# Kernel tuning notes

Measured on AMD Instinct MI355X. Metric: run time of the kernel, lower is better.

## Reference

```python
import jax, jax.numpy as jnp
import numpy as np
import math

NUM_BINS = 10
TAIL_BOUND = 5.0
FILTER_CHANNELS = 192
KERNEL_SIZE = 3
N_LAYERS = 3
HALF = 1
MIN_BIN = 1e-3
MIN_DERIV = 1e-3


def conv1d(x, w, b, dilation=1, groups=1, padding=0):
    # x: [B,C,T], w: [O, C//groups, K]
    y = jax.lax.conv_general_dilated(
        x, w, window_strides=(1,), padding=[(padding, padding)],
        rhs_dilation=(dilation,), dimension_numbers=('NCH', 'OIH', 'NCH'),
        feature_group_count=groups)
    return y + b[None, :, None]


def ln_channels(x, g, b, eps=1e-5):
    # LayerNorm over channel dim (VITS modules.LayerNorm)
    m = jnp.mean(x, axis=1, keepdims=True)
    v = jnp.mean((x - m) ** 2, axis=1, keepdims=True)
    return g[None, :, None] * (x - m) * jax.lax.rsqrt(v + eps) + b[None, :, None]


def rq_spline(x1, uw, uh, ud):
    # piecewise rational-quadratic transform with linear tails (Durkan et al.)
    # x1: [B,1,T]; uw,uh: [B,1,T,K]; ud: [B,1,T,K-1]
    K = NUM_BINS
    tb = TAIL_BOUND
    inside = (x1 >= -tb) & (x1 <= tb)

    const = math.log(math.exp(1.0 - MIN_DERIV) - 1.0)  # softplus^-1(1-min_d)
    ud = jnp.pad(ud, [(0, 0)] * (ud.ndim - 1) + [(1, 1)], constant_values=const)

    widths = jax.nn.softmax(uw, axis=-1)
    widths = MIN_BIN + (1.0 - MIN_BIN * K) * widths
    cumw = jnp.pad(jnp.cumsum(widths, -1), [(0, 0)] * (uw.ndim - 1) + [(1, 0)])
    cumw = 2.0 * tb * cumw - tb
    cumw = cumw.at[..., 0].set(-tb).at[..., -1].set(tb)
    widths = cumw[..., 1:] - cumw[..., :-1]

    heights = jax.nn.softmax(uh, axis=-1)
    heights = MIN_BIN + (1.0 - MIN_BIN * K) * heights
    cumh = jnp.pad(jnp.cumsum(heights, -1), [(0, 0)] * (uh.ndim - 1) + [(1, 0)])
    cumh = 2.0 * tb * cumh - tb
    cumh = cumh.at[..., 0].set(-tb).at[..., -1].set(tb)
    heights = cumh[..., 1:] - cumh[..., :-1]

    derivs = MIN_DERIV + jax.nn.softplus(ud)  # [..., K+1]

    xin = jnp.clip(x1, -tb, tb)  # clamp so out-of-range lanes stay finite
    locs = cumw.at[..., -1].add(1e-6)
    bin_idx = jnp.clip(jnp.sum((xin[..., None] >= locs).astype(jnp.int32), -1) - 1, 0, K - 1)

    def take(a):
        return jnp.take_along_axis(a, bin_idx[..., None], axis=-1)[..., 0]

    icw = take(cumw)
    iw = take(widths)
    ich = take(cumh)
    ih = take(heights)
    d_l = take(derivs[..., :-1])
    d_r = take(derivs[..., 1:])
    delta = ih / iw

    theta = (xin - icw) / iw
    t1m = theta * (1.0 - theta)
    numerator = ih * (delta * theta * theta + d_l * t1m)
    denominator = delta + (d_l + d_r - 2.0 * delta) * t1m
    y = ich + numerator / denominator
    dnum = (delta * delta) * (d_r * theta * theta + 2.0 * delta * t1m + d_l * (1.0 - theta) ** 2)
    lad = jnp.log(dnum) - 2.0 * jnp.log(denominator)

    out = jnp.where(inside, y, x1)       # linear tails: identity outside
    lad = jnp.where(inside, lad, 0.0)
    return out, lad


def reference(x, x_mask, pre_w, pre_b, sep_w, sep_b, pw_w, pw_b,
              ln1_g, ln1_b, ln2_g, ln2_b, proj_w, proj_b):
    x0, x1 = x[:, :HALF], x[:, HALF:]
    h = conv1d(x0, pre_w, pre_b)
    # DDSConv (dilated depth-separable conv stack), p_dropout=0
    for i in range(N_LAYERS):
        d = KERNEL_SIZE ** i
        pad = (KERNEL_SIZE * d - d) // 2
        y = conv1d(h * x_mask, sep_w[i], sep_b[i], dilation=d,
                   groups=FILTER_CHANNELS, padding=pad)
        y = jax.nn.gelu(ln_channels(y, ln1_g[i], ln1_b[i]), approximate=False)
        y = conv1d(y, pw_w[i], pw_b[i])
        y = jax.nn.gelu(ln_channels(y, ln2_g[i], ln2_b[i]), approximate=False)
        h = h + y
    h = h * x_mask
    h = conv1d(h, proj_w, proj_b) * x_mask  # [B, half*(3K-1), T]
    b, c, t = x0.shape
    h = h.reshape(b, c, -1, t).transpose(0, 1, 3, 2)  # [B, half, T, 3K-1]
    scale = math.sqrt(FILTER_CHANNELS)
    uw = h[..., :NUM_BINS] / scale
    uh = h[..., NUM_BINS:2 * NUM_BINS] / scale
    ud = h[..., 2 * NUM_BINS:]
    x1o, lad = rq_spline(x1, uw, uh, ud)
    out = jnp.concatenate([x0, x1o], axis=1) * x_mask
    logdet = jnp.sum(lad * x_mask, axis=(1, 2))
    return out, logdet


def setup_inputs() -> dict:
    key = jax.random.key(0)
    ks = jax.random.split(key, 8)
    B, T, C, L, K = 64, 4096, FILTER_CHANNELS, N_LAYERS, KERNEL_SIZE
    return {
        'x': jax.random.normal(ks[0], (B, 2, T), jnp.float32),
        'x_mask': jnp.ones((B, 1, T), jnp.float32),
        'pre_w': jax.random.normal(ks[1], (C, 1, 1), jnp.float32) * 0.1,
        'pre_b': jnp.zeros((C,), jnp.float32),
        'sep_w': jax.random.normal(ks[2], (L, C, 1, K), jnp.float32) * 0.1,
        'sep_b': jnp.zeros((L, C), jnp.float32),
        'pw_w': jax.random.normal(ks[3], (L, C, C, 1), jnp.float32) * (1.0 / np.sqrt(C).astype(np.float32)),
        'pw_b': jnp.zeros((L, C), jnp.float32),
        'ln1_g': jnp.ones((L, C), jnp.float32),
        'ln1_b': jnp.zeros((L, C), jnp.float32),
        'ln2_g': jnp.ones((L, C), jnp.float32),
        'ln2_b': jnp.zeros((L, C), jnp.float32),
        'proj_w': jax.random.normal(ks[4], (HALF * (3 * NUM_BINS - 1), C, 1), jnp.float32) * 0.01,
        'proj_b': jnp.zeros((HALF * (3 * NUM_BINS - 1),), jnp.float32),
    }
```

## Files before the change

### kernel.cpp

```cpp
#include <hip/hip_runtime.h>
#include <stdint.h>

#define TT_ 4096
#define CC_ 192
#define TILE_ 64
#define HALO_ 13
#define TW_ 90
#define HS_ 100
#define YTS_ 200
#define NT_ 512

typedef float f32x2 __attribute__((ext_vector_type(2)));
typedef float f32x4 __attribute__((ext_vector_type(4)));
typedef short s16x4 __attribute__((ext_vector_type(4)));
typedef short s16x8 __attribute__((ext_vector_type(8)));
typedef uint32_t ui32x2 __attribute__((ext_vector_type(2)));
typedef uint32_t ui32x4 __attribute__((ext_vector_type(4)));

__device__ __forceinline__ float bf2f(short s){
  uint32_t u = ((uint32_t)(uint16_t)s) << 16;
  float f; __builtin_memcpy(&f, &u, 4); return f;
}
__device__ __forceinline__ float bfhalf(uint32_t u, int hi){
  uint32_t v = hi ? (u & 0xFFFF0000u) : (u << 16);
  float f; __builtin_memcpy(&f, &v, 4); return f;
}
__device__ __forceinline__ short f2bf(float f){
  uint32_t u; __builtin_memcpy(&u, &f, 4);
  u += 0x7FFFu + ((u >> 16) & 1u);
  return (short)(u >> 16);
}
__device__ __forceinline__ uint32_t fbits(float f){
  uint32_t u; __builtin_memcpy(&u, &f, 4); return u;
}
__device__ __forceinline__ uint32_t pk_trunc(float lo, float hi){
  return __builtin_amdgcn_perm(fbits(hi), fbits(lo), 0x07060302u);
}
__device__ __forceinline__ uint32_t rne_u(float f){
  uint32_t u = fbits(f);
  return u + 0x7FFFu + ((u >> 16) & 1u);
}
__device__ __forceinline__ uint32_t pk_rne(float lo, float hi){
  return __builtin_amdgcn_perm(rne_u(hi), rne_u(lo), 0x07060302u);
}
__device__ __forceinline__ f32x2 pfma(f32x2 a, f32x2 b, f32x2 c){
  return __builtin_elementwise_fma(a, b, c);
}
__device__ __forceinline__ f32x2 gelu2(f32x2 x){
  f32x2 s = x*x;
  f32x2 t = pfma(s, f32x2{0.0713548162f,0.0713548162f}, f32x2{1.5957691216f,1.5957691216f});
  f32x2 p = x*t;
  f32x2 q = p * f32x2{-1.44269504089f,-1.44269504089f};
  f32x2 e; e[0] = __builtin_amdgcn_exp2f(q[0]); e[1] = __builtin_amdgcn_exp2f(q[1]);
  f32x2 d = e + f32x2{1.f,1.f};
  f32x2 r; r[0] = __builtin_amdgcn_rcpf(d[0]); r[1] = __builtin_amdgcn_rcpf(d[1]);
  return x*r;
}
__device__ __forceinline__ int ytix(int row, int col){
  int key = (row ^ (row >> 2)) & 3;
  return row*YTS_ + ((((col >> 3) ^ key) << 3) | (col & 7));
}

template<int D>
__device__ __forceinline__ void dw_pass(const short* __restrict__ Hs, short* __restrict__ YTs,
    const float* __restrict__ sw, const float* __restrict__ sb,
    int jlo, int jhi, int tid){
  constexpr int WO = (D==9) ? 16 : 8;
  constexpr int NU = (D==9) ? 20 : 12;
  for (int g = tid; g < 96*12; g += NT_){
    int cg = g % 96, jg = g / 96;
    int j0 = jg*8;
    if (j0 + 8 <= jlo || j0 >= jhi) continue;
    int c0 = cg*2;
    uint32_t wpa[NU], wpb[NU];
    {
      const uint32_t* ra = (const uint32_t*)(Hs + (c0+0)*HS_ + j0 - WO);
      const uint32_t* rb = (const uint32_t*)(Hs + (c0+1)*HS_ + j0 - WO);
      #pragma unroll
      for (int u = 0; u < NU/2; ++u){
        ui32x2 ta = *(const ui32x2*)(ra + u*2);
        ui32x2 tb = *(const ui32x2*)(rb + u*2);
        wpa[u*2] = ta[0]; wpa[u*2+1] = ta[1];
        wpb[u*2] = tb[0]; wpb[u*2+1] = tb[1];
      }
    }
    f32x2 wv0 = { sw[c0*3+0], sw[c0*3+3] };
    f32x2 wv1 = { sw[c0*3+1], sw[c0*3+4] };
    f32x2 wv2 = { sw[c0*3+2], sw[c0*3+5] };
    f32x2 bb2 = { sb[c0], sb[c0+1] };
    #pragma unroll
    for (int j = 0; j < 8; ++j){
      int h0 = WO + j - D, h1 = WO + j, h2 = WO + j + D;
      f32x2 t0 = { bfhalf(wpa[h0>>1], h0&1), bfhalf(wpb[h0>>1], h0&1) };
      f32x2 t1 = { bfhalf(wpa[h1>>1], h1&1), bfhalf(wpb[h1>>1], h1&1) };
      f32x2 t2 = { bfhalf(wpa[h2>>1], h2&1), bfhalf(wpb[h2>>1], h2&1) };
      f32x2 acc = pfma(wv0, t0, pfma(wv1, t1, pfma(wv2, t2, bb2)));
      *(uint32_t*)(YTs + ytix(j0+j, c0)) = pk_trunc(acc[0], acc[1]);
    }
  }
}

__device__ __forceinline__ void ln_stats(const short* __restrict__ YTs, float* __restrict__ SM,
                                         float* __restrict__ SR, int jlo, int jhi, int tid){
  if (tid < 384){
    int row = tid >> 2, qtr = tid & 3;
    if (row >= jlo && row < jhi){
      f32x2 s2 = {0.f,0.f}, q2 = {0.f,0.f};
      #pragma unroll
      for (int u=0;u<6;++u){
        ui32x4 w = *(const ui32x4*)(YTs + ytix(row, qtr*48 + u*8));
        #pragma unroll
        for (int k=0;k<4;++k){
          f32x2 pr = { bfhalf(w[k],0), bfhalf(w[k],1) };
          s2 += pr; q2 = pfma(pr, pr, q2);
        }
      }
      float s = s2[0]+s2[1], q = q2[0]+q2[1];
      s += __shfl_xor(s,1); q += __shfl_xor(q,1);
      s += __shfl_xor(s,2); q += __shfl_xor(q,2);
      if (qtr==0){
        float mean = s*(1.f/192.f);
        float var = fmaxf(q*(1.f/192.f) - mean*mean, 0.f);
        SM[row]=mean; SR[row]=rsqrtf(var+1e-5f);
      }
    }
  }
}

__global__ __launch_bounds__(512, 4)
void convflow_main(
    const float* __restrict__ x, const float* __restrict__ xmask,
    const float* __restrict__ pre_w, const float* __restrict__ pre_b,
    const float* __restrict__ sep_w, const float* __restrict__ sep_b,
    const float* __restrict__ pw_b,
    const float* __restrict__ ln1_g, const float* __restrict__ ln1_b,
    const float* __restrict__ ln2_g, const float* __restrict__ ln2_b,
    const float* __restrict__ proj_b,
    const short* __restrict__ Wbf, const short* __restrict__ Pbf,
    float* __restrict__ out, float* __restrict__ part)
{
  __shared__ __align__(16) char smem_raw[78592];
  float* MB = (float*)(smem_raw + 0);
  float* XB = (float*)(smem_raw + 640);
  float* SM = (float*)(smem_raw + 1024);
  float* SR = (float*)(smem_raw + 1408);
  short* H  = (short*)(smem_raw + 1792);
  short* YT = (short*)(smem_raw + 40192);
  float* HP = (float*)(smem_raw + 65792);

  const int tid = threadIdx.x;
  const int b = blockIdx.y, tile = blockIdx.x;
  const int t0 = tile*TILE_ - HALO_;

  for (int idx = tid; idx < 160; idx += NT_){
    int j = idx - 16; int t = t0 + j;
    float m = 0.f;
    if (j >= 0 && j < TW_ && t >= 0 && t < TT_) m = xmask[b*TT_ + t];
    MB[idx] = m;
  }
  if (tid < 96){
    int t = t0 + tid; float v = 0.f;
    if (tid < TW_ && t >= 0 && t < TT_) v = x[(b*2)*TT_ + t];
    XB[tid] = v;
  }
  __syncthreads();

  for (int g = tid; g < CC_*24; g += NT_){
    int jq = g % 24, c = g / 24;
    float w = pre_w[c], bb = pre_b[c];
    int j0 = jq*4;
    float v0 = (w*XB[j0+0] + bb)*MB[16+j0+0];
    float v1 = (w*XB[j0+1] + bb)*MB[16+j0+1];
    float v2 = (w*XB[j0+2] + bb)*MB[16+j0+2];
    float v3 = (w*XB[j0+3] + bb)*MB[16+j0+3];
    ui32x2 o; o[0] = pk_rne(v0, v1); o[1] = pk_rne(v2, v3);
    *(ui32x2*)(H + c*HS_ + j0) = o;
  }
  __syncthreads();

  #pragma unroll 1
  for (int li = 0; li < 3; ++li){
    const int jlo = (li==0) ? 1 : ((li==1) ? 4 : 13);
    const int jhi = (li==0) ? 89 : ((li==1) ? 86 : 77);
    const float* sw = sep_w + li*CC_*3;
    const float* sb = sep_b + li*CC_;

    if (li == 0)      dw_pass<1>(H, YT, sw, sb, jlo, jhi, tid);
    else if (li == 1) dw_pass<3>(H, YT, sw, sb, jlo, jhi, tid);
    else              dw_pass<9>(H, YT, sw, sb, jlo, jhi, tid);
    __syncthreads();

    ln_stats(YT, SM, SR, jlo, jhi, tid); __syncthreads();

    {
      const float* g1 = ln1_g + li*CC_;
      const float* b1 = ln1_b + li*CC_;
      for (int g = tid; g < 96*24; g += NT_){
        int ch = g % 24, row = g / 24;
        short* p = YT + ytix(row, ch*8);
        if (row >= jlo && row < jhi){
          float m = SM[row], r = SR[row];
          f32x2 r2 = {r, r}, nm2 = {-m, -m};
          f32x4 ga = *(const f32x4*)&g1[ch*8], gb = *(const f32x4*)&g1[ch*8+4];
          f32x4 ba = *(const f32x4*)&b1[ch*8], bb = *(const f32x4*)&b1[ch*8+4];
          ui32x4 v = *(ui32x4*)p;
          ui32x4 o;
          #pragma unroll
          for (int k=0;k<4;++k){
            f32x2 pr = { bfhalf(v[k],0), bfhalf(v[k],1) };
            f32x2 gk = (k<2) ? f32x2{ga[2*k], ga[2*k+1]} : f32x2{gb[2*k-4], gb[2*k-3]};
            f32x2 bk = (k<2) ? f32x2{ba[2*k], ba[2*k+1]} : f32x2{bb[2*k-4], bb[2*k-3]};
            f32x2 A = gk * r2;
            f32x2 B = pfma(A, nm2, bk);
            f32x2 val = pfma(pr, A, B);
            f32x2 gl = gelu2(val);
            o[k] = pk_trunc(gl[0], gl[1]);
          }
          *(ui32x4*)p = o;
        } else {
          ui32x4 z = {0u,0u,0u,0u};
          *(ui32x4*)p = z;
        }
      }
    }
    __syncthreads();

    {
      int w = tid >> 6, lane = tid & 63, l16 = lane & 15, q = lane >> 4;
      int Mh = w & 3, Nh = w >> 2;
      f32x4 acc[3][3];
      #pragma unroll
      for (int r=0;r<3;r++)
        #pragma unroll
        for (int s=0;s<3;s++){ f32x4 z = {0.f,0.f,0.f,0.f}; acc[r][s] = z; }
      const short* Wl = Wbf + li*CC_*CC_;
      #pragma unroll
      for (int kk=0;kk<6;++kk){
        s16x8 bv[3], av[3];
        #pragma unroll
        for (int s=0;s<3;++s)
          bv[s] = *(const s16x8*)&YT[ytix((Nh*3+s)*16 + l16, kk*32 + q*8)];
        #pragma unroll
        for (int r=0;r<3;++r)
          av[r] = *(const s16x8*)&Wl[((Mh*3+r)*16 + l16)*CC_ + kk*32 + q*8];
        #pragma unroll
        for (int r=0;r<3;++r)
          #pragma unroll
          for (int s=0;s<3;++s)
            acc[r][s] = __builtin_amdgcn_mfma_f32_16x16x32_bf16(av[r], bv[s], acc[r][s], 0, 0, 0);
      }
      __syncthreads();
      #pragma unroll
      for (int r=0;r<3;++r){
        int m0 = (Mh*3+r)*16 + q*4;
        f32x4 bias = *(const f32x4*)&pw_b[li*CC_ + m0];
        #pragma unroll
        for (int s=0;s<3;++s){
          int n = (Nh*3+s)*16 + l16;
          ui32x2 ov;
          ov[0] = pk_trunc(acc[r][s][0]+bias[0], acc[r][s][1]+bias[1]);
          ov[1] = pk_trunc(acc[r][s][2]+bias[2], acc[r][s][3]+bias[3]);
          *(ui32x2*)(YT + ytix(n, m0)) = ov;
        }
      }
      __syncthreads();
    }

    ln_stats(YT, SM, SR, jlo, jhi, tid); __syncthreads();

    {
      const float* g2 = ln2_g + li*CC_;
      const float* b2 = ln2_b + li*CC_;
      for (int g = tid; g < 24*48; g += NT_){
        int jq = g % 24, cq = g / 24;
        int j0 = jq*4, c0 = cq*4;
        if (j0 + 4 <= jlo || j0 >= jhi) continue;
        f32x4 mv = *(f32x4*)&SM[j0], rv = *(f32x4*)&SR[j0];
        f32x4 mk = *(f32x4*)&MB[16 + j0];
        f32x4 gv = *(const f32x4*)&g2[c0], bv = *(const f32x4*)&b2[c0];
        s16x4 yr[4];
        #pragma unroll
        for (int jj=0;jj<4;++jj) yr[jj] = *(s16x4*)(YT + ytix(j0+jj, c0));
        bool ok0 = (j0   >= jlo) && (j0   < jhi);
        bool ok1 = (j0+1 >= jlo) && (j0+1 < jhi);
        bool ok2 = (j0+2 >= jlo) && (j0+2 < jhi);
        bool ok3 = (j0+3 >= jlo) && (j0+3 < jhi);
        #pragma unroll
        for (int cc=0;cc<4;++cc){
          short* hp_ = H + (c0+cc)*HS_ + j0;
          ui32x2 hw = *(ui32x2*)hp_;
          f32x2 gcc = { gv[cc], gv[cc] }, bcc = { bv[cc], bv[cc] };
          ui32x2 ho;
          #pragma unroll
          for (int pp=0; pp<2; ++pp){
            int ja = pp*2, jb = ja+1;
            f32x2 pr = { bf2f(yr[ja][cc]), bf2f(yr[jb][cc]) };
            f32x2 A = f32x2{rv[ja], rv[jb]} * gcc;
            f32x2 B = pfma(A, f32x2{-mv[ja], -mv[jb]}, bcc);
            f32x2 val = pfma(pr, A, B);
            f32x2 gl = gelu2(val);
            f32x2 h2 = { bfhalf(hw[pp],0), bfhalf(hw[pp],1) };
            f32x2 hn = (h2 + gl) * f32x2{mk[ja], mk[jb]};
            bool oa = pp ? ok2 : ok0, ob = pp ? ok3 : ok1;
            float f0 = oa ? hn[0] : h2[0];
            float f1 = ob ? hn[1] : h2[1];
            ho[pp] = pk_rne(f0, f1);
          }
          *(ui32x2*)hp_ = ho;
        }
      }
    }
    __syncthreads();
  }

  {
    int w = tid >> 6;
    if (w < 4){
      int lane = tid & 63, l16 = lane & 15, q = lane >> 4;
      int mt = w >> 1, ntp = w & 1;
      f32x4 pacc[2];
      { f32x4 z = {0.f,0.f,0.f,0.f}; pacc[0] = z; pacc[1] = z; }
      #pragma unroll
      for (int kk=0;kk<6;++kk){
        s16x8 a = *(const s16x8*)&Pbf[(mt*16 + l16)*CC_ + kk*32 + q*8];
        #pragma unroll
        for (int s=0;s<2;++s){
          int n = (ntp*2+s)*16 + l16;
          s16x8 bvv;
          #pragma unroll
          for (int i=0;i<8;++i)
            bvv[i] = H[(kk*32 + q*8 + i)*HS_ + HALO_ + n];
          pacc[s] = __builtin_amdgcn_mfma_f32_16x16x32_bf16(a, bvv, pacc[s], 0, 0, 0);
        }
      }
      #pragma unroll
      for (int s=0;s<2;++s)
        #pragma unroll
        for (int e=0;e<4;e++){
          int m = mt*16 + q*4 + e;
          if (m < 29){
            int n = (ntp*2+s)*16 + l16;
            HP[n*33 + m] = (pacc[s][e] + proj_b[m]) * MB[16 + HALO_ + n];
          }
        }
    }
  }
  __syncthreads();

  if (tid < 64){
    const int n = tid;
    const int tg = tile*TILE_ + n;
    const float msk = MB[16 + HALO_ + n];
    const float* hp = &HP[n*33];
    const float inv_s = 0.07216878364870323f;
    float uw[10], uh[10], ud9[9];
    #pragma unroll
    for (int k=0;k<10;k++){ uw[k] = hp[k]*inv_s; uh[k] = hp[10+k]*inv_s; }
    #pragma unroll
    for (int k=0;k<9;k++) ud9[k] = hp[20+k];

    float cumw[11], cumh[11];
    {
      float mx = uw[0];
      #pragma unroll
      for (int k=1;k<10;k++) mx = fmaxf(mx, uw[k]);
      float ex[10]; float ss = 0.f;
      #pragma unroll
      for (int k=0;k<10;k++){ ex[k] = __expf(uw[k]-mx); ss += ex[k]; }
      float inv = 1.0f/ss;
      cumw[0] = -5.f; float cw = 0.f;
      #pragma unroll
      for (int k=0;k<10;k++){ float wk = 0.001f + 0.99f*(ex[k]*inv); cw += wk; cumw[k+1] = 10.f*cw - 5.f; }
      cumw[10] = 5.f;
    }
    {
      float mx = uh[0];
      #pragma unroll
      for (int k=1;k<10;k++) mx = fmaxf(mx, uh[k]);
      float ex[10]; float ss = 0.f;
      #pragma unroll
      for (int k=0;k<10;k++){ ex[k] = __expf(uh[k]-mx); ss += ex[k]; }
      float inv = 1.0f/ss;
      cumh[0] = -5.f; float ch = 0.f;
      #pragma unroll
      for (int k=0;k<10;k++){ float hk = 0.001f + 0.99f*(ex[k]*inv); ch += hk; cumh[k+1] = 10.f*ch - 5.f; }
      cumh[10] = 5.f;
    }
    float dv[11];
    dv[0] = 1.0f; dv[10] = 1.0f;
    #pragma unroll
    for (int k=0;k<9;k++){
      float u = ud9[k];
      float sp = (u > 15.f) ? u : log1pf(__expf(u));
      dv[k+1] = 0.001f + sp;
    }

    const float x1 = x[(b*2+1)*TT_ + tg];
    const float xin = fminf(fmaxf(x1, -5.f), 5.f);
    int cnt = 0;
    #pragma unroll
    for (int k=0;k<11;k++){
      float lk = cumw[k] + ((k==10) ? 1e-6f : 0.f);
      cnt += (xin >= lk) ? 1 : 0;
    }
    int bin = cnt - 1;
    bin = (bin < 0) ? 0 : ((bin > 9) ? 9 : bin);

    float icw=0.f, iw=1.f, ich=0.f, ih=1.f, dl=1.f, dr=1.f;
    #pragma unroll
    for (int k=0;k<10;k++){
      if (bin == k){
        icw = cumw[k]; iw = cumw[k+1]-cumw[k];
        ich = cumh[k]; ih = cumh[k+1]-cumh[k];
        dl = dv[k]; dr = dv[k+1];
      }
    }
    float delta = ih/iw;
    float th = (xin - icw)/iw;
    float t1m = th*(1.f-th);
    float num = ih*(delta*th*th + dl*t1m);
    float den = delta + (dl + dr - 2.f*delta)*t1m;
    float yv = ich + num/den;
    float omt = 1.f - th;
    float dnum = delta*delta*(dr*th*th + 2.f*delta*t1m + dl*omt*omt);
    float lad = logf(dnum) - 2.f*logf(den);
    bool inside = (x1 >= -5.f) && (x1 <= 5.f);
    float outv = inside ? yv : x1;
    float ladv = inside ? lad : 0.f;

    out[(b*2)*TT_ + tg]   = x[(b*2)*TT_ + tg] * msk;
    out[(b*2+1)*TT_ + tg] = outv * msk;

    float lsum = ladv * msk;
    #pragma unroll
    for (int off = 32; off > 0; off >>= 1) lsum += __shfl_xor(lsum, off);
    if (tid == 0) part[b*64 + tile] = lsum;
  }
}

__global__ void convflow_pre(const float* __restrict__ pw_w, const float* __restrict__ proj_w,
                             short* __restrict__ Wbf, short* __restrict__ Pbf){
  int idx = blockIdx.x*256 + threadIdx.x;
  if (idx < 110592) Wbf[idx] = f2bf(pw_w[idx]);
  if (idx < 32*192){
    int m = idx / 192, k = idx - m*192;
    Pbf[idx] = (m < 29) ? f2bf(proj_w[m*192 + k]) : (short)0;
  }
}

__global__ void convflow_logdet(const float* __restrict__ part, float* __restrict__ out){
  int bb = threadIdx.x;
  if (bb < 64){
    float s = 0.f;
    for (int k=0;k<64;k++) s += part[bb*64 + k];
    out[524288 + bb] = s;
  }
}

extern "C" void kernel_launch(void* const* d_in, const int* in_sizes, int n_in,
                              void* d_out, int out_size, void* d_ws, size_t ws_size,
                              hipStream_t stream) {
  const float* x      = (const float*)d_in[0];
  const float* xmask  = (const float*)d_in[1];
  const float* pre_w  = (const float*)d_in[2];
  const float* pre_b  = (const float*)d_in[3];
  const float* sep_w  = (const float*)d_in[4];
  const float* sep_b  = (const float*)d_in[5];
  const float* pw_w   = (const float*)d_in[6];
  const float* pw_b   = (const float*)d_in[7];
  const float* ln1_g  = (const float*)d_in[8];
  const float* ln1_b  = (const float*)d_in[9];
  const float* ln2_g  = (const float*)d_in[10];
  const float* ln2_b  = (const float*)d_in[11];
  const float* proj_w = (const float*)d_in[12];
  const float* proj_b = (const float*)d_in[13];

  short* Wbf = (short*)d_ws;
  short* Pbf = (short*)((char*)d_ws + 221184);
  float* part = (float*)((char*)d_ws + 233472);
  float* out = (float*)d_out;

  convflow_pre<<<432, 256, 0, stream>>>(pw_w, proj_w, Wbf, Pbf);
  dim3 grid(64, 64);
  convflow_main<<<grid, NT_, 0, stream>>>(x, xmask, pre_w, pre_b, sep_w, sep_b, pw_b,
                                          ln1_g, ln1_b, ln2_g, ln2_b, proj_b,
                                          Wbf, Pbf, out, part);
  convflow_logdet<<<1, 64, 0, stream>>>(part, out);
}
```

Measured before the change: 602.7 us.

## Run two tile contexts per 1024-thread block with staggered phase pipeline

Each block now runs two 512-thread sub-groups, each handling its own time tile with its own shared-memory context. The per-tile work is split into 25 phases separated by block-wide barriers, and the second sub-group lags three phases behind the first. The aim is for phases that use different units (MFMA GEMM, elementwise GELU/LN, global loads) to overlap inside one block. The cost is doubled shared memory per block (about 157KB), fewer resident blocks per CU, and barriers that tie both groups together while they run unequal phases.

Result: slower. 1.918 ms (+218.3%).

```diff
diff --git a/kernel.cpp b/kernel.cpp
--- a/kernel.cpp
+++ b/kernel.cpp
@@ -9,6 +9,9 @@
 #define HS_ 100
 #define YTS_ 200
 #define NT_ 512
+#define CTXB_ 78592
+#define STAG_ 3
+#define NP_ 25
 
 typedef float f32x2 __attribute__((ext_vector_type(2)));
 typedef float f32x4 __attribute__((ext_vector_type(4)));
@@ -64,10 +67,10 @@
 template<int D>
 __device__ __forceinline__ void dw_pass(const short* __restrict__ Hs, short* __restrict__ YTs,
     const float* __restrict__ sw, const float* __restrict__ sb,
-    int jlo, int jhi, int tid){
+    int jlo, int jhi, int stid){
   constexpr int WO = (D==9) ? 16 : 8;
   constexpr int NU = (D==9) ? 20 : 12;
-  for (int g = tid; g < 96*12; g += NT_){
+  for (int g = stid; g < 96*12; g += NT_){
     int cg = g % 96, jg = g / 96;
     int j0 = jg*8;
     if (j0 + 8 <= jlo || j0 >= jhi) continue;
@@ -101,9 +104,9 @@
 }
 
 __device__ __forceinline__ void ln_stats(const short* __restrict__ YTs, float* __restrict__ SM,
-                                         float* __restrict__ SR, int jlo, int jhi, int tid){
-  if (tid < 384){
-    int row = tid >> 2, qtr = tid & 3;
+                                         float* __restrict__ SR, int jlo, int jhi, int stid){
+  if (stid < 384){
+    int row = stid >> 2, qtr = stid & 3;
     if (row >= jlo && row < jhi){
       f32x2 s2 = {0.f,0.f}, q2 = {0.f,0.f};
       #pragma unroll
@@ -127,7 +130,7 @@
   }
 }
 
-__global__ __launch_bounds__(512, 4)
+__global__ __launch_bounds__(1024, 4)
 void convflow_main(
     const float* __restrict__ x, const float* __restrict__ xmask,
     const float* __restrict__ pre_w, const float* __restrict__ pre_b,
@@ -139,302 +142,299 @@
     const short* __restrict__ Wbf, const short* __restrict__ Pbf,
     float* __restrict__ out, float* __restrict__ part)
 {
-  __shared__ __align__(16) char smem_raw[78592];
-  float* MB = (float*)(smem_raw + 0);
-  float* XB = (float*)(smem_raw + 640);
-  float* SM = (float*)(smem_raw + 1024);
-  float* SR = (float*)(smem_raw + 1408);
-  short* H  = (short*)(smem_raw + 1792);
-  short* YT = (short*)(smem_raw + 40192);
-  float* HP = (float*)(smem_raw + 65792);
+  __shared__ __align__(16) char smem_raw[2*CTXB_];
 
   const int tid = threadIdx.x;
-  const int b = blockIdx.y, tile = blockIdx.x;
+  const int sid = tid >> 9, stid = tid & 511;
+  char* base = smem_raw + sid*CTXB_;
+  float* MB = (float*)(base + 0);
+  float* XB = (float*)(base + 640);
+  float* SM = (float*)(base + 1024);
+  float* SR = (float*)(base + 1408);
+  short* H  = (short*)(base + 1792);
+  short* YT = (short*)(base + 40192);
+  float* HP = (float*)(base + 65792);
+
+  const int b = blockIdx.y, tile = blockIdx.x*2 + sid;
   const int t0 = tile*TILE_ - HALO_;
 
-  for (int idx = tid; idx < 160; idx += NT_){
-    int j = idx - 16; int t = t0 + j;
-    float m = 0.f;
-    if (j >= 0 && j < TW_ && t >= 0 && t < TT_) m = xmask[b*TT_ + t];
-    MB[idx] = m;
-  }
-  if (tid < 96){
-    int t = t0 + tid; float v = 0.f;
-    if (tid < TW_ && t >= 0 && t < TT_) v = x[(b*2)*TT_ + t];
-    XB[tid] = v;
-  }
-  __syncthreads();
-
-  for (int g = tid; g < CC_*24; g += NT_){
-    int jq = g % 24, c = g / 24;
-    float w = pre_w[c], bb = pre_b[c];
-    int j0 = jq*4;
-    float v0 = (w*XB[j0+0] + bb)*MB[16+j0+0];
-    float v1 = (w*XB[j0+1] + bb)*MB[16+j0+1];
-    float v2 = (w*XB[j0+2] + bb)*MB[16+j0+2];
-    float v3 = (w*XB[j0+3] + bb)*MB[16+j0+3];
-    ui32x2 o; o[0] = pk_rne(v0, v1); o[1] = pk_rne(v2, v3);
-    *(ui32x2*)(H + c*HS_ + j0) = o;
-  }
-  __syncthreads();
+  f32x4 acc[3][3];
 
   #pragma unroll 1
-  for (int li = 0; li < 3; ++li){
-    const int jlo = (li==0) ? 1 : ((li==1) ? 4 : 13);
-    const int jhi = (li==0) ? 89 : ((li==1) ? 86 : 77);
-    const float* sw = sep_w + li*CC_*3;
-    const float* sb = sep_b + li*CC_;
-
-    if (li == 0)      dw_pass<1>(H, YT, sw, sb, jlo, jhi, tid);
-    else if (li == 1) dw_pass<3>(H, YT, sw, sb, jlo, jhi, tid);
-    else              dw_pass<9>(H, YT, sw, sb, jlo, jhi, tid);
-    __syncthreads();
-
-    ln_stats(YT, SM, SR, jlo, jhi, tid); __syncthreads();
-
-    {
-      const float* g1 = ln1_g + li*CC_;
-      const float* b1 = ln1_b + li*CC_;
-      for (int g = tid; g < 96*24; g += NT_){
-        int ch = g % 24, row = g / 24;
-        short* p = YT + ytix(row, ch*8);
-        if (row >= jlo && row < jhi){
-          float m = SM[row], r = SR[row];
-          f32x2 r2 = {r, r}, nm2 = {-m, -m};
-          f32x4 ga = *(const f32x4*)&g1[ch*8], gb = *(const f32x4*)&g1[ch*8+4];
-          f32x4 ba = *(const f32x4*)&b1[ch*8], bb = *(const f32x4*)&b1[ch*8+4];
-          ui32x4 v = *(ui32x4*)p;
-          ui32x4 o;
-          #pragma unroll
-          for (int k=0;k<4;++k){
-            f32x2 pr = { bfhalf(v[k],0), bfhalf(v[k],1) };
-            f32x2 gk = (k<2) ? f32x2{ga[2*k], ga[2*k+1]} : f32x2{gb[2*k-4], gb[2*k-3]};
-            f32x2 bk = (k<2) ? f32x2{ba[2*k], ba[2*k+1]} : f32x2{bb[2*k-4], bb[2*k-3]};
-            f32x2 A = gk * r2;
-            f32x2 B = pfma(A, nm2, bk);
-            f32x2 val = pfma(pr, A, B);
-            f32x2 gl = gelu2(val);
-            o[k] = pk_trunc(gl[0], gl[1]);
-          }
-          *(ui32x4*)p = o;
+  for (int step = 0; step < NP_ + STAG_; ++step){
+    const int ph = (sid == 0) ? step : step - STAG_;
+    if (ph >= 0 && ph < NP_){
+      if (ph == 0){
+        for (int idx = stid; idx < 160; idx += NT_){
+          int j = idx - 16; int t = t0 + j;
+          float m = 0.f;
+          if (j >= 0 && j < TW_ && t >= 0 && t < TT_) m = xmask[b*TT_ + t];
+          MB[idx] = m;
+        }
+        if (stid < 96){
+          int t = t0 + stid; float v = 0.f;
+          if (stid < TW_ && t >= 0 && t < TT_) v = x[(b*2)*TT_ + t];
+          XB[stid] = v;
+        }
+      } else if (ph == 1){
+        for (int g = stid; g < CC_*24; g += NT_){
+          int jq = g % 24, c = g / 24;
+          float w = pre_w[c], bb = pre_b[c];
+          int j0 = jq*4;
+          float v0 = (w*XB[j0+0] + bb)*MB[16+j0+0];
+          float v1 = (w*XB[j0+1] + bb)*MB[16+j0+1];
+          float v2 = (w*XB[j0+2] + bb)*MB[16+j0+2];
+          float v3 = (w*XB[j0+3] + bb)*MB[16+j0+3];
+          ui32x2 o; o[0] = pk_rne(v0, v1); o[1] = pk_rne(v2, v3);
+          *(ui32x2*)(H + c*HS_ + j0) = o;
+        }
+      } else if (ph < 23){
+        const int li = (ph-2)/7, sub = (ph-2)%7;
+        const int jlo = (li==0) ? 1 : ((li==1) ? 4 : 13);
+        const int jhi = (li==0) ? 89 : ((li==1) ? 86 : 77);
+        if (sub == 0){
+          const float* sw = sep_w + li*CC_*3;
+          const float* sb = sep_b + li*CC_;
+          if (li == 0)      dw_pass<1>(H, YT, sw, sb, jlo, jhi, stid);
+          else if (li == 1) dw_pass<3>(H, YT, sw, sb, jlo, jhi, stid);
+          else              dw_pass<9>(H, YT, sw, sb, jlo, jhi, stid);
+        } else if (sub == 1 || sub == 5){
+          ln_stats(YT, SM, SR, jlo, jhi, stid);
+        } else if (sub == 2){
+          const float* g1 = ln1_g + li*CC_;
+          const float* b1 = ln1_b + li*CC_;
+          for (int g = stid; g < 96*24; g += NT_){
+            int ch = g % 24, row = g / 24;
+            short* p = YT + ytix(row, ch*8);
+            if (row >= jlo && row < jhi){
+              float m = SM[row], r = SR[row];
+              f32x2 r2 = {r, r}, nm2 = {-m, -m};
+              f32x4 ga = *(const f32x4*)&g1[ch*8], gb = *(const f32x4*)&g1[ch*8+4];
+              f32x4 ba = *(const f32x4*)&b1[ch*8], bb = *(const f32x4*)&b1[ch*8+4];
+              ui32x4 v = *(ui32x4*)p;
+              ui32x4 o;
+              #pragma unroll
+              for (int k=0;k<4;++k){
+                f32x2 pr = { bfhalf(v[k],0), bfhalf(v[k],1) };
+                f32x2 gk = (k<2) ? f32x2{ga[2*k], ga[2*k+1]} : f32x2{gb[2*k-4], gb[2*k-3]};
+                f32x2 bk = (k<2) ? f32x2{ba[2*k], ba[2*k+1]} : f32x2{bb[2*k-4], bb[2*k-3]};
+                f32x2 A = gk * r2;
+                f32x2 B = pfma(A, nm2, bk);
+                f32x2 val = pfma(pr, A, B);
+                f32x2 gl = gelu2(val);
+                o[k] = pk_trunc(gl[0], gl[1]);
+              }
+              *(ui32x4*)p = o;
+            } else {
+              ui32x4 z = {0u,0u,0u,0u};
+              *(ui32x4*)p = z;
+            }
+          }
+        } else if (sub == 3){
+          int w = stid >> 6, lane = stid & 63, l16 = lane & 15, q = lane >> 4;
+          int Mh = w & 3, Nh = w >> 2;
+          #pragma unroll
+          for (int r=0;r<3;r++)
+            #pragma unroll
+            for (int s=0;s<3;s++){ f32x4 z = {0.f,0.f,0.f,0.f}; acc[r][s] = z; }
+          const short* Wl = Wbf + li*CC_*CC_;
+          #pragma unroll
+          for (int kk=0;kk<6;++kk){
+            s16x8 bv[3], av[3];
+            #pragma unroll
+            for (int s=0;s<3;++s)
+              bv[s] = *(const s16x8*)&YT[ytix((Nh*3+s)*16 + l16, kk*32 + q*8)];
+            #pragma unroll
+            for (int r=0;r<3;++r)
+              av[r] = *(const s16x8*)&Wl[((Mh*3+r)*16 + l16)*CC_ + kk*32 + q*8];
+            #pragma unroll
+            for (int r=0;r<3;++r)
+              #pragma unroll
+              for (int s=0;s<3;++s)
+                acc[r][s] = __builtin_amdgcn_mfma_f32_16x16x32_bf16(av[r], bv[s], acc[r][s], 0, 0, 0);
+          }
+        } else if (sub == 4){
+          int w = stid >> 6, lane = stid & 63, l16 = lane & 15, q = lane >> 4;
+          int Mh = w & 3, Nh = w >> 2;
+          #pragma unroll
+          for (int r=0;r<3;++r){
+            int m0 = (Mh*3+r)*16 + q*4;
+            f32x4 bias = *(const f32x4*)&pw_b[li*CC_ + m0];
+            #pragma unroll
+            for (int s=0;s<3;++s){
+              int n = (Nh*3+s)*16 + l16;
+              ui32x2 ov;
+              ov[0] = pk_trunc(acc[r][s][0]+bias[0], acc[r][s][1]+bias[1]);
+              ov[1] = pk_trunc(acc[r][s][2]+bias[2], acc[r][s][3]+bias[3]);
+              *(ui32x2*)(YT + ytix(n, m0)) = ov;
+            }
+          }
         } else {
-          ui32x4 z = {0u,0u,0u,0u};
-          *(ui32x4*)p = z;
+          const float* g2 = ln2_g + li*CC_;
+          const float* b2 = ln2_b + li*CC_;
+          for (int g = stid; g < 24*48; g += NT_){
+            int jq = g % 24, cq = g / 24;
+            int j0 = jq*4, c0 = cq*4;
+            if (j0 + 4 <= jlo || j0 >= jhi) continue;
+            f32x4 mv = *(f32x4*)&SM[j0], rv = *(f32x4*)&SR[j0];
+            f32x4 mk = *(f32x4*)&MB[16 + j0];
+            f32x4 gv = *(const f32x4*)&g2[c0], bv = *(const f32x4*)&b2[c0];
+            s16x4 yr[4];
+            #pragma unroll
+            for (int jj=0;jj<4;++jj) yr[jj] = *(s16x4*)(YT + ytix(j0+jj, c0));
+            bool ok0 = (j0   >= jlo) && (j0   < jhi);
+            bool ok1 = (j0+1 >= jlo) && (j0+1 < jhi);
+            bool ok2 = (j0+2 >= jlo) && (j0+2 < jhi);
+            bool ok3 = (j0+3 >= jlo) && (j0+3 < jhi);
+            #pragma unroll
+            for (int cc=0;cc<4;++cc){
+              short* hp_ = H + (c0+cc)*HS_ + j0;
+              ui32x2 hw = *(ui32x2*)hp_;
+              f32x2 gcc = { gv[cc], gv[cc] }, bcc = { bv[cc], bv[cc] };
+              ui32x2 ho;
+              #pragma unroll
+              for (int pp=0; pp<2; ++pp){
+                int ja = pp*2, jb = ja+1;
+                f32x2 pr = { bf2f(yr[ja][cc]), bf2f(yr[jb][cc]) };
+                f32x2 A = f32x2{rv[ja], rv[jb]} * gcc;
+                f32x2 B = pfma(A, f32x2{-mv[ja], -mv[jb]}, bcc);
+                f32x2 val = pfma(pr, A, B);
+                f32x2 gl = gelu2(val);
+                f32x2 h2 = { bfhalf(hw[pp],0), bfhalf(hw[pp],1) };
+                f32x2 hn = (h2 + gl) * f32x2{mk[ja], mk[jb]};
+                bool oa = pp ? ok2 : ok0, ob = pp ? ok3 : ok1;
+                float f0 = oa ? hn[0] : h2[0];
+                float f1 = ob ? hn[1] : h2[1];
+                ho[pp] = pk_rne(f0, f1);
+              }
+              *(ui32x2*)hp_ = ho;
+            }
+          }
+        }
+      } else if (ph == 23){
+        int w = stid >> 6;
+        if (w < 4){
+          int lane = stid & 63, l16 = lane & 15, q = lane >> 4;
+          int mt = w >> 1, ntp = w & 1;
+          f32x4 pacc[2];
+          { f32x4 z = {0.f,0.f,0.f,0.f}; pacc[0] = z; pacc[1] = z; }
+          #pragma unroll
+          for (int kk=0;kk<6;++kk){
+            s16x8 a = *(const s16x8*)&Pbf[(mt*16 + l16)*CC_ + kk*32 + q*8];
+            #pragma unroll
+            for (int s=0;s<2;++s){
+              int n = (ntp*2+s)*16 + l16;
+              s16x8 bvv;
+              #pragma unroll
+              for (int i=0;i<8;++i)
+                bvv[i] = H[(kk*32 + q*8 + i)*HS_ + HALO_ + n];
+              pacc[s] = __builtin_amdgcn_mfma_f32_16x16x32_bf16(a, bvv, pacc[s], 0, 0, 0);
+            }
+          }
+          #pragma unroll
+          for (int s=0;s<2;++s)
+            #pragma unroll
+            for (int e=0;e<4;e++){
+              int m = mt*16 + q*4 + e;
+              if (m < 29){
+                int n = (ntp*2+s)*16 + l16;
+                HP[n*33 + m] = (pacc[s][e] + proj_b[m]) * MB[16 + HALO_ + n];
+              }
+            }
+        }
+      } else {
+        if (stid < 64){
+          const int n = stid;
+          const int tg = tile*TILE_ + n;
+          const float msk = MB[16 + HALO_ + n];
+          const float* hp = &HP[n*33];
+          const float inv_s = 0.07216878364870323f;
+          float uw[10], uh[10], ud9[9];
+          #pragma unroll
+          for (int k=0;k<10;k++){ uw[k] = hp[k]*inv_s; uh[k] = hp[10+k]*inv_s; }
+          #pragma unroll
+          for (int k=0;k<9;k++) ud9[k] = hp[20+k];
+
+          float cumw[11], cumh[11];
+          {
+            float mx = uw[0];
+            #pragma unroll
+            for (int k=1;k<10;k++) mx = fmaxf(mx, uw[k]);
+            float ex[10]; float ss = 0.f;
+            #pragma unroll
+            for (int k=0;k<10;k++){ ex[k] = __expf(uw[k]-mx); ss += ex[k]; }
+            float inv = 1.0f/ss;
+            cumw[0] = -5.f; float cw = 0.f;
+            #pragma unroll
+            for (int k=0;k<10;k++){ float wk = 0.001f + 0.99f*(ex[k]*inv); cw += wk; cumw[k+1] = 10.f*cw - 5.f; }
+            cumw[10] = 5.f;
+          }
+          {
+            float mx = uh[0];
+            #pragma unroll
+            for (int k=1;k<10;k++) mx = fmaxf(mx, uh[k]);
+            float ex[10]; float ss = 0.f;
+            #pragma unroll
+            for (int k=0;k<10;k++){ ex[k] = __expf(uh[k]-mx); ss += ex[k]; }
+            float inv = 1.0f/ss;
+            cumh[0] = -5.f; float ch = 0.f;
+            #pragma unroll
+            for (int k=0;k<10;k++){ float hk = 0.001f + 0.99f*(ex[k]*inv); ch += hk; cumh[k+1] = 10.f*ch - 5.f; }
+            cumh[10] = 5.f;
+          }
+          float dv[11];
+          dv[0] = 1.0f; dv[10] = 1.0f;
+          #pragma unroll
+          for (int k=0;k<9;k++){
+            float u = ud9[k];
+            float sp = (u > 15.f) ? u : log1pf(__expf(u));
+            dv[k+1] = 0.001f + sp;
+          }
+
+          const float x1 = x[(b*2+1)*TT_ + tg];
+          const float xin = fminf(fmaxf(x1, -5.f), 5.f);
+          int cnt = 0;
+          #pragma unroll
+          for (int k=0;k<11;k++){
+            float lk = cumw[k] + ((k==10) ? 1e-6f : 0.f);
+            cnt += (xin >= lk) ? 1 : 0;
+          }
+          int bin = cnt - 1;
+          bin = (bin < 0) ? 0 : ((bin > 9) ? 9 : bin);
+
+          float icw=0.f, iw=1.f, ich=0.f, ih=1.f, dl=1.f, dr=1.f;
+          #pragma unroll
+          for (int k=0;k<10;k++){
+            if (bin == k){
+              icw = cumw[k]; iw = cumw[k+1]-cumw[k];
+              ich = cumh[k]; ih = cumh[k+1]-cumh[k];
+              dl = dv[k]; dr = dv[k+1];
+            }
+          }
+          float delta = ih/iw;
+          float th = (xin - icw)/iw;
+          float t1m = th*(1.f-th);
+          float num = ih*(delta*th*th + dl*t1m);
+          float den = delta + (dl + dr - 2.f*delta)*t1m;
+          float yv = ich + num/den;
+          float omt = 1.f - th;
+          float dnum = delta*delta*(dr*th*th + 2.f*delta*t1m + dl*omt*omt);
+          float lad = logf(dnum) - 2.f*logf(den);
+          bool inside = (x1 >= -5.f) && (x1 <= 5.f);
+          float outv = inside ? yv : x1;
+          float ladv = inside ? lad : 0.f;
+
+          out[(b*2)*TT_ + tg]   = x[(b*2)*TT_ + tg] * msk;
+          out[(b*2+1)*TT_ + tg] = outv * msk;
+
+          float lsum = ladv * msk;
+          #pragma unroll
+          for (int off = 32; off > 0; off >>= 1) lsum += __shfl_xor(lsum, off);
+          if (stid == 0) part[b*64 + tile] = lsum;
         }
       }
     }
     __syncthreads();
-
-    {
-      int w = tid >> 6, lane = tid & 63, l16 = lane & 15, q = lane >> 4;
-      int Mh = w & 3, Nh = w >> 2;
-      f32x4 acc[3][3];
-      #pragma unroll
-      for (int r=0;r<3;r++)
-        #pragma unroll
-        for (int s=0;s<3;s++){ f32x4 z = {0.f,0.f,0.f,0.f}; acc[r][s] = z; }
-      const short* Wl = Wbf + li*CC_*CC_;
-      #pragma unroll
-      for (int kk=0;kk<6;++kk){
-        s16x8 bv[3], av[3];
-        #pragma unroll
-        for (int s=0;s<3;++s)
-          bv[s] = *(const s16x8*)&YT[ytix((Nh*3+s)*16 + l16, kk*32 + q*8)];
-        #pragma unroll
-        for (int r=0;r<3;++r)
-          av[r] = *(const s16x8*)&Wl[((Mh*3+r)*16 + l16)*CC_ + kk*32 + q*8];
-        #pragma unroll
-        for (int r=0;r<3;++r)
-          #pragma unroll
-          for (int s=0;s<3;++s)
-            acc[r][s] = __builtin_amdgcn_mfma_f32_16x16x32_bf16(av[r], bv[s], acc[r][s], 0, 0, 0);
-      }
-      __syncthreads();
-      #pragma unroll
-      for (int r=0;r<3;++r){
-        int m0 = (Mh*3+r)*16 + q*4;
-        f32x4 bias = *(const f32x4*)&pw_b[li*CC_ + m0];
-        #pragma unroll
-        for (int s=0;s<3;++s){
-          int n = (Nh*3+s)*16 + l16;
-          ui32x2 ov;
-          ov[0] = pk_trunc(acc[r][s][0]+bias[0], acc[r][s][1]+bias[1]);
-          ov[1] = pk_trunc(acc[r][s][2]+bias[2], acc[r][s][3]+bias[3]);
-          *(ui32x2*)(YT + ytix(n, m0)) = ov;
-        }
-      }
-      __syncthreads();
-    }
-
-    ln_stats(YT, SM, SR, jlo, jhi, tid); __syncthreads();
-
-    {
-      const float* g2 = ln2_g + li*CC_;
-      const float* b2 = ln2_b + li*CC_;
-      for (int g = tid; g < 24*48; g += NT_){
-        int jq = g % 24, cq = g / 24;
-        int j0 = jq*4, c0 = cq*4;
-        if (j0 + 4 <= jlo || j0 >= jhi) continue;
-        f32x4 mv = *(f32x4*)&SM[j0], rv = *(f32x4*)&SR[j0];
-        f32x4 mk = *(f32x4*)&MB[16 + j0];
-        f32x4 gv = *(const f32x4*)&g2[c0], bv = *(const f32x4*)&b2[c0];
-        s16x4 yr[4];
-        #pragma unroll
-        for (int jj=0;jj<4;++jj) yr[jj] = *(s16x4*)(YT + ytix(j0+jj, c0));
-        bool ok0 = (j0   >= jlo) && (j0   < jhi);
-        bool ok1 = (j0+1 >= jlo) && (j0+1 < jhi);
-        bool ok2 = (j0+2 >= jlo) && (j0+2 < jhi);
-        bool ok3 = (j0+3 >= jlo) && (j0+3 < jhi);
-        #pragma unroll
-        for (int cc=0;cc<4;++cc){
-          short* hp_ = H + (c0+cc)*HS_ + j0;
-          ui32x2 hw = *(ui32x2*)hp_;
-          f32x2 gcc = { gv[cc], gv[cc] }, bcc = { bv[cc], bv[cc] };
-          ui32x2 ho;
-          #pragma unroll
-          for (int pp=0; pp<2; ++pp){
-            int ja = pp*2, jb = ja+1;
-            f32x2 pr = { bf2f(yr[ja][cc]), bf2f(yr[jb][cc]) };
-            f32x2 A = f32x2{rv[ja], rv[jb]} * gcc;
-            f32x2 B = pfma(A, f32x2{-mv[ja], -mv[jb]}, bcc);
-            f32x2 val = pfma(pr, A, B);
-            f32x2 gl = gelu2(val);
-            f32x2 h2 = { bfhalf(hw[pp],0), bfhalf(hw[pp],1) };
-            f32x2 hn = (h2 + gl) * f32x2{mk[ja], mk[jb]};
-            bool oa = pp ? ok2 : ok0, ob = pp ? ok3 : ok1;
-            float f0 = oa ? hn[0] : h2[0];
-            float f1 = ob ? hn[1] : h2[1];
-            ho[pp] = pk_rne(f0, f1);
-          }
-          *(ui32x2*)hp_ = ho;
-        }
-      }
-    }
-    __syncthreads();
-  }
-
-  {
-    int w = tid >> 6;
-    if (w < 4){
-      int lane = tid & 63, l16 = lane & 15, q = lane >> 4;
-      int mt = w >> 1, ntp = w & 1;
-      f32x4 pacc[2];
-      { f32x4 z = {0.f,0.f,0.f,0.f}; pacc[0] = z; pacc[1] = z; }
-      #pragma unroll
-      for (int kk=0;kk<6;++kk){
-        s16x8 a = *(const s16x8*)&Pbf[(mt*16 + l16)*CC_ + kk*32 + q*8];
-        #pragma unroll
-        for (int s=0;s<2;++s){
-          int n = (ntp*2+s)*16 + l16;
-          s16x8 bvv;
-          #pragma unroll
-          for (int i=0;i<8;++i)
-            bvv[i] = H[(kk*32 + q*8 + i)*HS_ + HALO_ + n];
-          pacc[s] = __builtin_amdgcn_mfma_f32_16x16x32_bf16(a, bvv, pacc[s], 0, 0, 0);
-        }
-      }
-      #pragma unroll
-      for (int s=0;s<2;++s)
-        #pragma unroll
-        for (int e=0;e<4;e++){
-          int m = mt*16 + q*4 + e;
-          if (m < 29){
-            int n = (ntp*2+s)*16 + l16;
-            HP[n*33 + m] = (pacc[s][e] + proj_b[m]) * MB[16 + HALO_ + n];
-          }
-        }
-    }
-  }
-  __syncthreads();
-
-  if (tid < 64){
-    const int n = tid;
-    const int tg = tile*TILE_ + n;
-    const float msk = MB[16 + HALO_ + n];
-    const float* hp = &HP[n*33];
-    const float inv_s = 0.07216878364870323f;
-    float uw[10], uh[10], ud9[9];
-    #pragma unroll
-    for (int k=0;k<10;k++){ uw[k] = hp[k]*inv_s; uh[k] = hp[10+k]*inv_s; }
-    #pragma unroll
-    for (int k=0;k<9;k++) ud9[k] = hp[20+k];
-
-    float cumw[11], cumh[11];
-    {
-      float mx = uw[0];
-      #pragma unroll
-      for (int k=1;k<10;k++) mx = fmaxf(mx, uw[k]);
-      float ex[10]; float ss = 0.f;
-      #pragma unroll
-      for (int k=0;k<10;k++){ ex[k] = __expf(uw[k]-mx); ss += ex[k]; }
-      float inv = 1.0f/ss;
-      cumw[0] = -5.f; float cw = 0.f;
-      #pragma unroll
-      for (int k=0;k<10;k++){ float wk = 0.001f + 0.99f*(ex[k]*inv); cw += wk; cumw[k+1] = 10.f*cw - 5.f; }
-      cumw[10] = 5.f;
-    }
-    {
-      float mx = uh[0];
-      #pragma unroll
-      for (int k=1;k<10;k++) mx = fmaxf(mx, uh[k]);
-      float ex[10]; float ss = 0.f;
-      #pragma unroll
-      for (int k=0;k<10;k++){ ex[k] = __expf(uh[k]-mx); ss += ex[k]; }
-      float inv = 1.0f/ss;
-      cumh[0] = -5.f; float ch = 0.f;
-      #pragma unroll
-      for (int k=0;k<10;k++){ float hk = 0.001f + 0.99f*(ex[k]*inv); ch += hk; cumh[k+1] = 10.f*ch - 5.f; }
-      cumh[10] = 5.f;
-    }
-    float dv[11];
-    dv[0] = 1.0f; dv[10] = 1.0f;
-    #pragma unroll
-    for (int k=0;k<9;k++){
-      float u = ud9[k];
-      float sp = (u > 15.f) ? u : log1pf(__expf(u));
-      dv[k+1] = 0.001f + sp;
-    }
-
-    const float x1 = x[(b*2+1)*TT_ + tg];
-    const float xin = fminf(fmaxf(x1, -5.f), 5.f);
-    int cnt = 0;
-    #pragma unroll
-    for (int k=0;k<11;k++){
-      float lk = cumw[k] + ((k==10) ? 1e-6f : 0.f);
-      cnt += (xin >= lk) ? 1 : 0;
-    }
-    int bin = cnt - 1;
-    bin = (bin < 0) ? 0 : ((bin > 9) ? 9 : bin);
-
-    float icw=0.f, iw=1.f, ich=0.f, ih=1.f, dl=1.f, dr=1.f;
-    #pragma unroll
-    for (int k=0;k<10;k++){
-      if (bin == k){
-        icw = cumw[k]; iw = cumw[k+1]-cumw[k];
-        ich = cumh[k]; ih = cumh[k+1]-cumh[k];
-        dl = dv[k]; dr = dv[k+1];
-      }
-    }
-    float delta = ih/iw;
-    float th = (xin - icw)/iw;
-    float t1m = th*(1.f-th);
-    float num = ih*(delta*th*th + dl*t1m);
-    float den = delta + (dl + dr - 2.f*delta)*t1m;
-    float yv = ich + num/den;
-    float omt = 1.f - th;
-    float dnum = delta*delta*(dr*th*th + 2.f*delta*t1m + dl*omt*omt);
-    float lad = logf(dnum) - 2.f*logf(den);
-    bool inside = (x1 >= -5.f) && (x1 <= 5.f);
-    float outv = inside ? yv : x1;
-    float ladv = inside ? lad : 0.f;
-
-    out[(b*2)*TT_ + tg]   = x[(b*2)*TT_ + tg] * msk;
-    out[(b*2+1)*TT_ + tg] = outv * msk;
-
-    float lsum = ladv * msk;
-    #pragma unroll
-    for (int off = 32; off > 0; off >>= 1) lsum += __shfl_xor(lsum, off);
-    if (tid == 0) part[b*64 + tile] = lsum;
   }
 }
 
@@ -481,9 +481,9 @@
   float* out = (float*)d_out;
 
   convflow_pre<<<432, 256, 0, stream>>>(pw_w, proj_w, Wbf, Pbf);
-  dim3 grid(64, 64);
-  convflow_main<<<grid, NT_, 0, stream>>>(x, xmask, pre_w, pre_b, sep_w, sep_b, pw_b,
-                                          ln1_g, ln1_b, ln2_g, ln2_b, proj_b,
-                                          Wbf, Pbf, out, part);
+  dim3 grid(32, 64);
+  convflow_main<<<grid, 1024, 0, stream>>>(x, xmask, pre_w, pre_b, sep_w, sep_b, pw_b,
+                                           ln1_g, ln1_b, ln2_g, ln2_b, proj_b,
+                                           Wbf, Pbf, out, part);
   convflow_logdet<<<1, 64, 0, stream>>>(part, out);
 }
```
